# Performance work log

Measured on AMD Instinct MI355X. Metric: run time of the kernel, lower is better.

Reference implementation:

```python
import jax, jax.numpy as jnp
import numpy as np
from jax import lax

KERNEL = 15
IGNORE = 255


def setup_inputs() -> dict:
    key = jax.random.key(0)
    k1, k2 = jax.random.split(key)
    B, C, H, W = 32, 2, 480, 864
    logits = jax.random.normal(k1, (B, C, H, W), dtype=jnp.float32)
    labels = jax.random.randint(k2, (B, H, W), 0, 2, dtype=jnp.int32)
    return {"logits": logits, "labels": labels}


def _boundary_edgemap(labels):
    # labels: [B, H, W] int32 with values in {0, 1, IGNORE}
    lbl = labels.astype(jnp.int32)
    # np_label = label*255, with ignore pixels set to 0 (matches cv2 path)
    np_label = jnp.where(lbl == IGNORE, 0, lbl * 255)
    win = (1, KERNEL, KERNEL)
    strides = (1, 1, 1)
    # cv2.erode with ones kernel == 15x15 min filter (border value +inf -> pad 255)
    erosion = lax.reduce_window(np_label, jnp.int32(255), lax.min, win, strides, "SAME")
    # cv2.dilate == 15x15 max filter (border value -inf -> pad 0)
    dilation = lax.reduce_window(np_label, jnp.int32(0), lax.max, win, strides, "SAME")
    boundary = dilation - erosion  # >0 exactly on the morphological boundary band
    edgemap = jnp.where(boundary > 0, lbl, IGNORE)
    edgemap = jnp.where(lbl == IGNORE, IGNORE, edgemap)
    return edgemap


def reference(logits, labels):
    # logits: [B, C, H, W] log-probabilities, labels: [B, H, W]
    edgemap = _boundary_edgemap(labels)  # [B, H, W]
    valid = edgemap != IGNORE
    tgt = jnp.where(valid, edgemap, 0)  # safe index for ignored pixels
    # gather logits[b, tgt, h, w] -> [B, H, W]
    picked = jnp.take_along_axis(logits, tgt[:, None, :, :], axis=1)[:, 0]
    # NLLLoss with ignore_index: mean of -logp over valid pixels
    n_valid = jnp.maximum(jnp.sum(valid), 1)
    loss = -jnp.sum(jnp.where(valid, picked, 0.0)) / n_valid.astype(logits.dtype)
    return loss
```

## Files before the change

### kernel.cpp

```cpp
#include <hip/hip_runtime.h>


namespace {
constexpr int B_ = 32;
constexpr int H_ = 480;
constexpr int W_ = 864;
constexpr int NW = 27;
constexpr int NMASK = B_ * H_ * NW;
constexpr int SROWS = 50;
constexpr int NSTRIP = 10;
constexpr int NWAVE = B_ * NW * NSTRIP;
constexpr int NBLK_B = NWAVE / 4;
constexpr size_t OFF_IGN = 2u << 20;
constexpr size_t OFF_PART = 4u << 20;
}

extern "C" __global__ __launch_bounds__(256)
void bl_bitpack(const int* __restrict__ labels,
                unsigned* __restrict__ Am, unsigned* __restrict__ Im)
{
  const int t = blockIdx.x * 256 + threadIdx.x;
  const int4* p = (const int4*)(labels + (size_t)t * 32);
  unsigned a = 0, ig = 0;
#pragma unroll
  for (int k = 0; k < 8; ++k) {
    const int4 v = p[k];
    a  |= ((v.x == 1)   ? 1u : 0u) << (4 * k)     | ((v.y == 1)   ? 2u : 0u) << (4 * k)
       |  ((v.z == 1)   ? 4u : 0u) << (4 * k)     | ((v.w == 1)   ? 8u : 0u) << (4 * k);
    ig |= ((v.x == 255) ? 1u : 0u) << (4 * k)     | ((v.y == 255) ? 2u : 0u) << (4 * k)
       |  ((v.z == 255) ? 4u : 0u) << (4 * k)     | ((v.w == 255) ? 8u : 0u) << (4 * k);
  }
  Am[t] = a;
  Im[t] = ig;
}

__device__ __forceinline__ unsigned hwin(unsigned w0, unsigned w1, unsigned w2) {
  unsigned long long L = ((unsigned long long)w1 << 32) | w0;
  unsigned long long R = ((unsigned long long)w2 << 32) | w1;
  L |= L << 1; L |= L << 2; L |= L << 4;
  R |= R >> 1; R |= R >> 2; R |= R >> 4;
  return (unsigned)(L >> 32) | (unsigned)R;
}

__device__ __forceinline__ unsigned vwin(unsigned x) {
  unsigned u = x, d = x;
  u |= __shfl_up(u, 1, 64);  u |= __shfl_up(u, 2, 64);  u |= __shfl_up(u, 4, 64);
  d |= __shfl_down(d, 1, 64); d |= __shfl_down(d, 2, 64); d |= __shfl_down(d, 4, 64);
  return u | d;
}

extern "C" __global__ __launch_bounds__(256)
void bl_main(const float* __restrict__ logits,
             const unsigned* __restrict__ Am, const unsigned* __restrict__ Im,
             float2* __restrict__ partials)
{
  const int tid = threadIdx.x;
  const int lane = tid & 63;
  const int wid = blockIdx.x * 4 + (tid >> 6);
  const int b = wid / (NW * NSTRIP);
  const int rem = wid - b * (NW * NSTRIP);
  const int dc = rem / NSTRIP;
  const int s = rem - dc * NSTRIP;

  const int gr = SROWS * s - 7 + lane;
  const bool inrow = (gr >= 0) && (gr < H_);
  const bool out_lane = (lane >= 7) && (lane <= 56) && (gr < H_);

  unsigned A0 = 0, A1 = 0, A2 = 0, Ic = 0;
  if (inrow) {
    const size_t rbase = ((size_t)b * H_ + gr) * NW + dc;
    A1 = Am[rbase];
    Ic = Im[rbase];
    if (dc > 0) A0 = Am[rbase - 1];
    if (dc < NW - 1) A2 = Am[rbase + 1];
  }
  const unsigned N0 = (inrow && dc > 0) ? ~A0 : 0u;
  const unsigned N1 = inrow ? ~A1 : 0u;
  const unsigned N2 = (inrow && dc < NW - 1) ? ~A2 : 0u;

  const unsigned hA = hwin(A0, A1, A2);
  const unsigned hN = hwin(N0, N1, N2);
  const unsigned vA = vwin(hA);
  const unsigned vN = vwin(hN);

  unsigned valid = out_lane ? (vA & vN & ~Ic) : 0u;

  float lsum = 0.f;
  unsigned lcnt = 0;
  if (out_lane) {
    const size_t off = ((size_t)b * 2 * H_ + gr) * W_ + dc * 32;
    const float4* p0 = (const float4*)(logits + off);
    const float4* p1 = (const float4*)(logits + off + (size_t)H_ * W_);
    float c0[32], c1[32];
#pragma unroll
    for (int k = 0; k < 8; ++k) {
      const float4 u0 = p0[k], u1 = p1[k];
      c0[4 * k] = u0.x; c0[4 * k + 1] = u0.y; c0[4 * k + 2] = u0.z; c0[4 * k + 3] = u0.w;
      c1[4 * k] = u1.x; c1[4 * k + 1] = u1.y; c1[4 * k + 2] = u1.z; c1[4 * k + 3] = u1.w;
    }
    lcnt = __popc(valid);
#pragma unroll
    for (int k = 0; k < 32; ++k) {
      const bool vb = (valid >> k) & 1u;
      const float pick = ((A1 >> k) & 1u) ? c1[k] : c0[k];
      lsum += vb ? pick : 0.f;
    }
  }

#pragma unroll
  for (int off = 32; off > 0; off >>= 1) {
    lsum += __shfl_down(lsum, off, 64);
    lcnt += __shfl_down(lcnt, off, 64);
  }
  if (lane == 0) partials[wid] = make_float2(lsum, (float)lcnt);
}

extern "C" __global__ __launch_bounds__(1024)
void bl_final(const float2* __restrict__ partials, float* __restrict__ out)
{
  __shared__ double red_s[16];
  __shared__ double red_c[16];
  const int tid = threadIdx.x;
  double s = 0.0, cc = 0.0;
  for (int i = tid; i < NWAVE; i += 1024) {
    const float2 p = partials[i];
    s += (double)p.x;
    cc += (double)p.y;
  }
#pragma unroll
  for (int off = 32; off > 0; off >>= 1) {
    s += __shfl_down(s, off, 64);
    cc += __shfl_down(cc, off, 64);
  }
  const int wave = tid >> 6;
  if ((tid & 63) == 0) { red_s[wave] = s; red_c[wave] = cc; }
  __syncthreads();
  if (tid == 0) {
    double ts = 0.0, tc = 0.0;
#pragma unroll
    for (int i = 0; i < 16; ++i) { ts += red_s[i]; tc += red_c[i]; }
    if (tc < 1.0) tc = 1.0;
    out[0] = (float)(-ts / tc);
  }
}

extern "C" void kernel_launch(void* const* d_in, const int* in_sizes, int n_in,
                              void* d_out, int out_size, void* d_ws, size_t ws_size,
                              hipStream_t stream)
{
  const float* logits = (const float*)d_in[0];
  const int* labels = (const int*)d_in[1];
  float* out = (float*)d_out;
  unsigned* Am = (unsigned*)d_ws;
  unsigned* Im = (unsigned*)((char*)d_ws + OFF_IGN);
  float2* partials = (float2*)((char*)d_ws + OFF_PART);

  bl_bitpack<<<NMASK / 256, 256, 0, stream>>>(labels, Am, Im);
  bl_main<<<NBLK_B, 256, 0, stream>>>(logits, Am, Im, partials);
  bl_final<<<1, 1024, 0, stream>>>(partials, out);
}
```

Baseline: 204.3 us.

## Split morphology and logits gather into separate kernels with coalesced float4 streaming

The morphology step moves into its own kernel, which writes a valid-pixel bitmask and per-wave counts. A new gather kernel streams the logits with fully coalesced float4 loads per thread and selects values using the mask. Before, each lane read 128 contiguous bytes per channel row, so global accesses across a wave were strided. The cost is one extra kernel launch plus a mask write and re-read, and every logits element is now loaded, including those outside the old halo window.

```diff
diff --git a/kernel.cpp b/kernel.cpp
--- a/kernel.cpp
+++ b/kernel.cpp
@@ -9,10 +9,15 @@
 constexpr int NMASK = B_ * H_ * NW;
 constexpr int SROWS = 50;
 constexpr int NSTRIP = 10;
-constexpr int NWAVE = B_ * NW * NSTRIP;
-constexpr int NBLK_B = NWAVE / 4;
-constexpr size_t OFF_IGN = 2u << 20;
-constexpr size_t OFF_PART = 4u << 20;
+constexpr int NWAVE_M = B_ * NW * NSTRIP;
+constexpr int NBLK_M = NWAVE_M / 4;
+constexpr int NF4 = B_ * 2 * H_ * W_ / 4;
+constexpr int NBLK_G = NF4 / 1024;
+constexpr int NWAVE_G = NBLK_G * 4;
+constexpr size_t OFF_IGN  = 2u << 20;
+constexpr size_t OFF_VAL  = 4u << 20;
+constexpr size_t OFF_CNT  = 6u << 20;
+constexpr size_t OFF_SUM  = 7u << 20;
 }
 
 extern "C" __global__ __launch_bounds__(256)
@@ -25,10 +30,10 @@
 #pragma unroll
   for (int k = 0; k < 8; ++k) {
     const int4 v = p[k];
-    a  |= ((v.x == 1)   ? 1u : 0u) << (4 * k)     | ((v.y == 1)   ? 2u : 0u) << (4 * k)
-       |  ((v.z == 1)   ? 4u : 0u) << (4 * k)     | ((v.w == 1)   ? 8u : 0u) << (4 * k);
-    ig |= ((v.x == 255) ? 1u : 0u) << (4 * k)     | ((v.y == 255) ? 2u : 0u) << (4 * k)
-       |  ((v.z == 255) ? 4u : 0u) << (4 * k)     | ((v.w == 255) ? 8u : 0u) << (4 * k);
+    a  |= ((v.x == 1)   ? 1u : 0u) << (4 * k) | ((v.y == 1)   ? 2u : 0u) << (4 * k)
+       |  ((v.z == 1)   ? 4u : 0u) << (4 * k) | ((v.w == 1)   ? 8u : 0u) << (4 * k);
+    ig |= ((v.x == 255) ? 1u : 0u) << (4 * k) | ((v.y == 255) ? 2u : 0u) << (4 * k)
+       |  ((v.z == 255) ? 4u : 0u) << (4 * k) | ((v.w == 255) ? 8u : 0u) << (4 * k);
   }
   Am[t] = a;
   Im[t] = ig;
@@ -50,9 +55,8 @@
 }
 
 extern "C" __global__ __launch_bounds__(256)
-void bl_main(const float* __restrict__ logits,
-             const unsigned* __restrict__ Am, const unsigned* __restrict__ Im,
-             float2* __restrict__ partials)
+void bl_morph(const unsigned* __restrict__ Am, const unsigned* __restrict__ Im,
+              unsigned* __restrict__ Vm, float* __restrict__ cnt_part)
 {
   const int tid = threadIdx.x;
   const int lane = tid & 63;
@@ -67,8 +71,9 @@
   const bool out_lane = (lane >= 7) && (lane <= 56) && (gr < H_);
 
   unsigned A0 = 0, A1 = 0, A2 = 0, Ic = 0;
+  size_t rbase = 0;
   if (inrow) {
-    const size_t rbase = ((size_t)b * H_ + gr) * NW + dc;
+    rbase = ((size_t)b * H_ + gr) * NW + dc;
     A1 = Am[rbase];
     Ic = Im[rbase];
     if (dc > 0) A0 = Am[rbase - 1];
@@ -78,55 +83,61 @@
   const unsigned N1 = inrow ? ~A1 : 0u;
   const unsigned N2 = (inrow && dc < NW - 1) ? ~A2 : 0u;
 
-  const unsigned hA = hwin(A0, A1, A2);
-  const unsigned hN = hwin(N0, N1, N2);
-  const unsigned vA = vwin(hA);
-  const unsigned vN = vwin(hN);
+  const unsigned vA = vwin(hwin(A0, A1, A2));
+  const unsigned vN = vwin(hwin(N0, N1, N2));
+  const unsigned valid = out_lane ? (vA & vN & ~Ic) : 0u;
 
-  unsigned valid = out_lane ? (vA & vN & ~Ic) : 0u;
+  if (out_lane) Vm[rbase] = valid;
 
+  unsigned lcnt = __popc(valid);
+#pragma unroll
+  for (int off = 32; off > 0; off >>= 1) lcnt += __shfl_down(lcnt, off, 64);
+  if (lane == 0) cnt_part[wid] = (float)lcnt;
+}
+
+extern "C" __global__ __launch_bounds__(256)
+void bl_gather(const float* __restrict__ logits,
+               const unsigned* __restrict__ Am, const unsigned* __restrict__ Vm,
+               float* __restrict__ sum_part)
+{
+  const int tid = threadIdx.x;
   float lsum = 0.f;
-  unsigned lcnt = 0;
-  if (out_lane) {
-    const size_t off = ((size_t)b * 2 * H_ + gr) * W_ + dc * 32;
-    const float4* p0 = (const float4*)(logits + off);
-    const float4* p1 = (const float4*)(logits + off + (size_t)H_ * W_);
-    float c0[32], c1[32];
 #pragma unroll
-    for (int k = 0; k < 8; ++k) {
-      const float4 u0 = p0[k], u1 = p1[k];
-      c0[4 * k] = u0.x; c0[4 * k + 1] = u0.y; c0[4 * k + 2] = u0.z; c0[4 * k + 3] = u0.w;
-      c1[4 * k] = u1.x; c1[4 * k + 1] = u1.y; c1[4 * k + 2] = u1.z; c1[4 * k + 3] = u1.w;
-    }
-    lcnt = __popc(valid);
+  for (int it = 0; it < 4; ++it) {
+    const int g = blockIdx.x * 1024 + it * 256 + tid;
+    const float4 v = *(const float4*)(logits + (size_t)g * 4);
+    const int row = g / 216;
+    const int col4 = g - row * 216;
+    const int col = col4 * 4;
+    const int b = row / 960;
+    const int remr = row - b * 960;
+    const int c = remr / 480;
+    const int h = remr - c * 480;
+    const size_t mi = ((size_t)b * H_ + h) * NW + (col >> 5);
+    const unsigned vm = Vm[mi];
+    const unsigned am = Am[mi];
+    const unsigned want = c ? (vm & am) : (vm & ~am);
+    const unsigned sel = (want >> (col & 31)) & 0xFu;
+    lsum += (sel & 1u) ? v.x : 0.f;
+    lsum += (sel & 2u) ? v.y : 0.f;
+    lsum += (sel & 4u) ? v.z : 0.f;
+    lsum += (sel & 8u) ? v.w : 0.f;
+  }
 #pragma unroll
-    for (int k = 0; k < 32; ++k) {
-      const bool vb = (valid >> k) & 1u;
-      const float pick = ((A1 >> k) & 1u) ? c1[k] : c0[k];
-      lsum += vb ? pick : 0.f;
-    }
-  }
-
-#pragma unroll
-  for (int off = 32; off > 0; off >>= 1) {
-    lsum += __shfl_down(lsum, off, 64);
-    lcnt += __shfl_down(lcnt, off, 64);
-  }
-  if (lane == 0) partials[wid] = make_float2(lsum, (float)lcnt);
+  for (int off = 32; off > 0; off >>= 1) lsum += __shfl_down(lsum, off, 64);
+  if ((tid & 63) == 0) sum_part[blockIdx.x * 4 + (tid >> 6)] = lsum;
 }
 
 extern "C" __global__ __launch_bounds__(1024)
-void bl_final(const float2* __restrict__ partials, float* __restrict__ out)
+void bl_final(const float* __restrict__ cnt_part,
+              const float* __restrict__ sum_part, float* __restrict__ out)
 {
   __shared__ double red_s[16];
   __shared__ double red_c[16];
   const int tid = threadIdx.x;
   double s = 0.0, cc = 0.0;
-  for (int i = tid; i < NWAVE; i += 1024) {
-    const float2 p = partials[i];
-    s += (double)p.x;
-    cc += (double)p.y;
-  }
+  for (int i = tid; i < NWAVE_G; i += 1024) s += (double)sum_part[i];
+  for (int i = tid; i < NWAVE_M; i += 1024) cc += (double)cnt_part[i];
 #pragma unroll
   for (int off = 32; off > 0; off >>= 1) {
     s += __shfl_down(s, off, 64);
@@ -153,9 +164,12 @@
   float* out = (float*)d_out;
   unsigned* Am = (unsigned*)d_ws;
   unsigned* Im = (unsigned*)((char*)d_ws + OFF_IGN);
-  float2* partials = (float2*)((char*)d_ws + OFF_PART);
+  unsigned* Vm = (unsigned*)((char*)d_ws + OFF_VAL);
+  float* cnt_part = (float*)((char*)d_ws + OFF_CNT);
+  float* sum_part = (float*)((char*)d_ws + OFF_SUM);
 
   bl_bitpack<<<NMASK / 256, 256, 0, stream>>>(labels, Am, Im);
-  bl_main<<<NBLK_B, 256, 0, stream>>>(logits, Am, Im, partials);
-  bl_final<<<1, 1024, 0, stream>>>(partials, out);
+  bl_morph<<<NBLK_M, 256, 0, stream>>>(Am, Im, Vm, cnt_part);
+  bl_gather<<<NBLK_G, 256, 0, stream>>>(logits, Am, Vm, sum_part);
+  bl_final<<<1, 1024, 0, stream>>>(cnt_part, sum_part, out);
 }
```

Result: slower. 211.8 us (+3.6%).
